# Performance work log

Hardware: AMD Instinct MI355X
Metric: run time of the kernel (lower is better)

Reference implementation:

```python
import jax, jax.numpy as jnp
import numpy as np

PATCH_SIZE = 16  # init_kwargs patch_size


def setup_inputs() -> dict:
    key = jax.random.key(0)
    k1, k2, k3 = jax.random.split(key, 3)
    B, C, H, W = 128, 3, 224, 224
    n_points = int(H * W * 0.5 / PATCH_SIZE ** 2)  # 98
    imgs = jax.random.normal(k1, (B, C, H, W), dtype=jnp.float32)
    points_x = jax.random.randint(k2, (B, n_points), 0, H - PATCH_SIZE + 1, dtype=jnp.int32)
    points_y = jax.random.randint(k3, (B, n_points), 0, W - PATCH_SIZE + 1, dtype=jnp.int32)
    return {"imgs": imgs, "points_x": points_x, "points_y": points_y}


def reference(imgs, points_x, points_y):
    # imgs: [B, C, H, W]; points_x/points_y: [B, N] top-left corners of P x P patches to zero.
    B, C, H, W = imgs.shape
    P = PATCH_SIZE
    off = jnp.arange(P, dtype=points_x.dtype)
    b = jnp.arange(B)[:, None, None, None]                       # [B,1,1,1]
    xs = points_x[:, :, None, None] + off[None, None, :, None]    # [B,N,P,1]
    ys = points_y[:, :, None, None] + off[None, None, None, :]    # [B,N,1,P]
    # Build occlusion mask once with a single scatter, then apply across channels.
    mask = jnp.zeros((B, H, W), dtype=jnp.bool_).at[b, xs, ys].set(True)  # [B,H,W]
    return jnp.where(mask[:, None, :, :], jnp.zeros((), imgs.dtype), imgs)
```

## Files before the change

kernel.cpp:

```cpp
#include <hip/hip_runtime.h>

#define BB 128
#define CC 3
#define HH 224
#define WW 224
#define PP 16

__global__ void occl_scatter_mask(unsigned char* __restrict__ mask,
                                  const int* __restrict__ px,
                                  const int* __restrict__ py,
                                  int total, int N) {
    int tid = blockIdx.x * blockDim.x + threadIdx.x;
    if (tid >= total) return;
    int j = tid & (PP - 1);
    int i = (tid >> 4) & (PP - 1);
    int p = tid >> 8;
    int b = p / N;
    int x = px[p];
    int y = py[p];
    mask[(size_t)b * (HH * WW) + (size_t)(x + i) * WW + (y + j)] = 1;
}

__global__ void occl_apply(float4* __restrict__ out,
                           const float4* __restrict__ imgs,
                           const unsigned int* __restrict__ mask32,
                           int total4) {
    int idx = blockIdx.x * blockDim.x + threadIdx.x;
    if (idx >= total4) return;
    const int W4 = WW / 4;
    int w4 = idx % W4;
    int t  = idx / W4;
    int h  = t % HH;
    int bc = t / HH;
    int b  = bc / CC;
    unsigned int m = mask32[(size_t)b * (HH * WW / 4) + h * W4 + w4];
    float4 v = imgs[idx];
    if (m) {
        if (m & 0x000000FFu) v.x = 0.f;
        if (m & 0x0000FF00u) v.y = 0.f;
        if (m & 0x00FF0000u) v.z = 0.f;
        if (m & 0xFF000000u) v.w = 0.f;
    }
    out[idx] = v;
}

__global__ void occl_copy(float4* __restrict__ out,
                          const float4* __restrict__ in, int total4) {
    int idx = blockIdx.x * blockDim.x + threadIdx.x;
    if (idx < total4) out[idx] = in[idx];
}

__global__ void occl_zero_patches(float* __restrict__ out,
                                  const int* __restrict__ px,
                                  const int* __restrict__ py,
                                  int total, int N) {
    int tid = blockIdx.x * blockDim.x + threadIdx.x;
    if (tid >= total) return;
    int j = tid & (PP - 1);
    int i = (tid >> 4) & (PP - 1);
    int t = tid >> 8;
    int c = t % CC;
    int p = t / CC;
    int b = p / N;
    int x = px[p];
    int y = py[p];
    size_t off = (((size_t)b * CC + c) * HH + (x + i)) * (size_t)WW + (y + j);
    out[off] = 0.f;
}

extern "C" void kernel_launch(void* const* d_in, const int* in_sizes, int n_in,
                              void* d_out, int out_size, void* d_ws, size_t ws_size,
                              hipStream_t stream) {
    const float* imgs = (const float*)d_in[0];
    const int*   px   = (const int*)d_in[1];
    const int*   py   = (const int*)d_in[2];
    float*       out  = (float*)d_out;

    const int N        = in_sizes[1] / BB;
    const int nPatches = BB * N;
    const size_t maskBytes = (size_t)BB * HH * WW;

    if (ws_size >= maskBytes) {
        hipMemsetAsync(d_ws, 0, maskBytes, stream);

        int totalScatter = nPatches * PP * PP;
        int blks = (totalScatter + 255) / 256;
        occl_scatter_mask<<<blks, 256, 0, stream>>>(
            (unsigned char*)d_ws, px, py, totalScatter, N);

        int total4 = out_size / 4;
        blks = (total4 + 255) / 256;
        occl_apply<<<blks, 256, 0, stream>>>(
            (float4*)out, (const float4*)imgs, (const unsigned int*)d_ws, total4);
    } else {
        int total4 = out_size / 4;
        int blks = (total4 + 255) / 256;
        occl_copy<<<blks, 256, 0, stream>>>((float4*)out, (const float4*)imgs, total4);

        int totalZero = nPatches * CC * PP * PP;
        blks = (totalZero + 255) / 256;
        occl_zero_patches<<<blks, 256, 0, stream>>>(out, px, py, totalZero, N);
    }
}
```

Baseline: 147.2 us.

## Fuse mask build and apply into one kernel with shared-memory row bitmasks

Replaces the memset, global byte-mask scatter and apply kernels with a single kernel. Each block rebuilds a per-image bitmask of occluded pixels in shared memory using atomicOr on 32-bit words, then streams its chunk of the image through float4 loads and stores. This removes the global mask traffic, the memset and two extra launches, at the cost of each of the 7 blocks per image redundantly rebuilding the same mask. The chunk size depends on the fixed image shape dividing evenly by 7*256.

```diff
diff --git a/kernel.cpp b/kernel.cpp
--- a/kernel.cpp
+++ b/kernel.cpp
@@ -6,66 +6,55 @@
 #define WW 224
 #define PP 16
 
-__global__ void occl_scatter_mask(unsigned char* __restrict__ mask,
-                                  const int* __restrict__ px,
-                                  const int* __restrict__ py,
-                                  int total, int N) {
-    int tid = blockIdx.x * blockDim.x + threadIdx.x;
-    if (tid >= total) return;
-    int j = tid & (PP - 1);
-    int i = (tid >> 4) & (PP - 1);
-    int p = tid >> 8;
-    int b = p / N;
-    int x = px[p];
-    int y = py[p];
-    mask[(size_t)b * (HH * WW) + (size_t)(x + i) * WW + (y + j)] = 1;
-}
+#define W4 (WW / 4)
+#define PER_IMG4 (CC * HH * W4)
+#define NCHUNK 7
+#define NWORDS (HH * 7)
 
-__global__ void occl_apply(float4* __restrict__ out,
-                           const float4* __restrict__ imgs,
-                           const unsigned int* __restrict__ mask32,
-                           int total4) {
-    int idx = blockIdx.x * blockDim.x + threadIdx.x;
-    if (idx >= total4) return;
-    const int W4 = WW / 4;
-    int w4 = idx % W4;
-    int t  = idx / W4;
-    int h  = t % HH;
-    int bc = t / HH;
-    int b  = bc / CC;
-    unsigned int m = mask32[(size_t)b * (HH * WW / 4) + h * W4 + w4];
-    float4 v = imgs[idx];
-    if (m) {
-        if (m & 0x000000FFu) v.x = 0.f;
-        if (m & 0x0000FF00u) v.y = 0.f;
-        if (m & 0x00FF0000u) v.z = 0.f;
-        if (m & 0xFF000000u) v.w = 0.f;
+__global__ __launch_bounds__(256) void occl_fused(
+        float4* __restrict__ out, const float4* __restrict__ imgs,
+        const int* __restrict__ px, const int* __restrict__ py, int N) {
+    __shared__ unsigned int rowbits[NWORDS];
+    const int t = threadIdx.x;
+    const int b = blockIdx.y;
+
+    for (int i = t; i < NWORDS; i += 256) rowbits[i] = 0u;
+    __syncthreads();
+
+    const int nrow = N * PP;
+    for (int r = t; r < nrow; r += 256) {
+        int p = r >> 4;
+        int i = r & (PP - 1);
+        int x = px[b * N + p] + i;
+        int y = py[b * N + p];
+        unsigned long long mm = 0xFFFFull << (y & 31);
+        int w0 = x * 7 + (y >> 5);
+        atomicOr(&rowbits[w0], (unsigned int)mm);
+        unsigned int hi = (unsigned int)(mm >> 32);
+        if (hi) atomicOr(&rowbits[w0 + 1], hi);
     }
-    out[idx] = v;
-}
+    __syncthreads();
 
-__global__ void occl_copy(float4* __restrict__ out,
-                          const float4* __restrict__ in, int total4) {
-    int idx = blockIdx.x * blockDim.x + threadIdx.x;
-    if (idx < total4) out[idx] = in[idx];
-}
-
-__global__ void occl_zero_patches(float* __restrict__ out,
-                                  const int* __restrict__ px,
-                                  const int* __restrict__ py,
-                                  int total, int N) {
-    int tid = blockIdx.x * blockDim.x + threadIdx.x;
-    if (tid >= total) return;
-    int j = tid & (PP - 1);
-    int i = (tid >> 4) & (PP - 1);
-    int t = tid >> 8;
-    int c = t % CC;
-    int p = t / CC;
-    int b = p / N;
-    int x = px[p];
-    int y = py[p];
-    size_t off = (((size_t)b * CC + c) * HH + (x + i)) * (size_t)WW + (y + j);
-    out[off] = 0.f;
+    const int chunk = PER_IMG4 / NCHUNK;
+    int base = blockIdx.x * chunk;
+    const float4* __restrict__ src = imgs + (size_t)b * PER_IMG4;
+    float4* __restrict__ dst = out + (size_t)b * PER_IMG4;
+#pragma unroll 3
+    for (int k = 0; k < chunk / 256; ++k) {
+        int f = base + k * 256 + t;
+        int w4 = f % W4;
+        int hh = (f / W4) % HH;
+        unsigned int word = rowbits[hh * 7 + (w4 >> 3)];
+        unsigned int m4 = (word >> ((w4 & 7) * 4)) & 0xFu;
+        float4 v = src[f];
+        if (m4) {
+            if (m4 & 1u) v.x = 0.f;
+            if (m4 & 2u) v.y = 0.f;
+            if (m4 & 4u) v.z = 0.f;
+            if (m4 & 8u) v.w = 0.f;
+        }
+        dst[f] = v;
+    }
 }
 
 extern "C" void kernel_launch(void* const* d_in, const int* in_sizes, int n_in,
@@ -76,29 +65,9 @@
     const int*   py   = (const int*)d_in[2];
     float*       out  = (float*)d_out;
 
-    const int N        = in_sizes[1] / BB;
-    const int nPatches = BB * N;
-    const size_t maskBytes = (size_t)BB * HH * WW;
+    const int N = in_sizes[1] / BB;
 
-    if (ws_size >= maskBytes) {
-        hipMemsetAsync(d_ws, 0, maskBytes, stream);
-
-        int totalScatter = nPatches * PP * PP;
-        int blks = (totalScatter + 255) / 256;
-        occl_scatter_mask<<<blks, 256, 0, stream>>>(
-            (unsigned char*)d_ws, px, py, totalScatter, N);
-
-        int total4 = out_size / 4;
-        blks = (total4 + 255) / 256;
-        occl_apply<<<blks, 256, 0, stream>>>(
-            (float4*)out, (const float4*)imgs, (const unsigned int*)d_ws, total4);
-    } else {
-        int total4 = out_size / 4;
-        int blks = (total4 + 255) / 256;
-        occl_copy<<<blks, 256, 0, stream>>>((float4*)out, (const float4*)imgs, total4);
-
-        int totalZero = nPatches * CC * PP * PP;
-        blks = (totalZero + 255) / 256;
-        occl_zero_patches<<<blks, 256, 0, stream>>>(out, px, py, totalZero, N);
-    }
+    dim3 grid(NCHUNK, BB);
+    occl_fused<<<grid, 256, 0, stream>>>(
+        (float4*)out, (const float4*)imgs, px, py, N);
 }
```

Result: faster. 144.0 us (-2.2%).
